# Optimization experiments

Measured on AMD Instinct MI355X. Metric: run time of the kernel, lower is better.

The kernel has to match this reference:

```python
import jax, jax.numpy as jnp
import numpy as np

N_NODES = 50000
E_DIM = 128
H_DIM = 256
OUT_DIM = 2
N_EDGES = 800000
NEG_SLOPE = 0.01  # nn.LeakyReLU default


def gcn_conv(x, W, b, src, dst, n):
    """PyG GCNConv: h = x @ W; add self-loops; sym-normalized scatter-add; + bias."""
    h = x @ W  # [N, H]
    loop = jnp.arange(n, dtype=src.dtype)
    s = jnp.concatenate([src, loop])
    d = jnp.concatenate([dst, loop])
    w = jnp.ones_like(s, dtype=h.dtype)
    deg = jax.ops.segment_sum(w, d, num_segments=n)  # in-degree incl. self-loop
    dis = jnp.where(deg > 0, jax.lax.rsqrt(deg), jnp.zeros_like(deg))
    norm = dis[s] * dis[d]  # [E+N]
    msg = h[s] * norm[:, None]  # gather + scale
    out = jax.ops.segment_sum(msg, d, num_segments=n)  # scatter-add to targets
    return out + b


def setup_inputs() -> dict:
    key = jax.random.key(0)
    ks = jax.random.split(key, 12)
    inp = {
        "mask_feature": jax.random.normal(ks[0], (N_NODES, E_DIM), jnp.float32),
        "feature": jax.random.normal(ks[1], (N_NODES, E_DIM), jnp.float32),
        "edge_index": jax.random.randint(ks[2], (2, N_EDGES), 0, N_NODES, jnp.int64 if jax.config.jax_enable_x64 else jnp.int32),
        "edge_type": jax.random.randint(ks[3], (N_EDGES,), 0, 2, jnp.int64 if jax.config.jax_enable_x64 else jnp.int32),
        # learned parameters
        "W_in": jax.random.normal(ks[4], (E_DIM, H_DIM), jnp.float32) * 0.05,
        "b_in": jnp.zeros((H_DIM,), jnp.float32),
        "Wg1": jax.random.normal(ks[5], (H_DIM, H_DIM), jnp.float32) * 0.05,
        "bg1": jnp.zeros((H_DIM,), jnp.float32),
        "Wg2": jax.random.normal(ks[6], (H_DIM, H_DIM), jnp.float32) * 0.05,
        "bg2": jnp.zeros((H_DIM,), jnp.float32),
        "W_out": jax.random.normal(ks[7], (H_DIM, OUT_DIM), jnp.float32) * 0.05,
        "b_out": jnp.zeros((OUT_DIM,), jnp.float32),
    }
    return inp


def reference(mask_feature, feature, edge_index, edge_type,
              W_in, b_in, Wg1, bg1, Wg2, bg2, W_out, b_out):
    src, dst = edge_index[0], edge_index[1]
    n = mask_feature.shape[0]
    # main branch
    x = jax.nn.leaky_relu(mask_feature @ W_in + b_in, NEG_SLOPE)
    x = gcn_conv(x, Wg1, bg1, src, dst, n)
    # dropout is identity at inference
    x = gcn_conv(x, Wg2, bg2, src, dst, n)
    x = x @ W_out + b_out  # [N, out_dim]
    # mask branch
    m = jax.nn.leaky_relu((feature - mask_feature) @ W_in + b_in, NEG_SLOPE)
    m = m @ W_out + b_out  # [N, out_dim]
    return x * m
```

## Files before the change

### kernel.cpp

```cpp
#include <hip/hip_runtime.h>


#define NEG_SLOPE 0.01f
constexpr int HD = 256;
constexpr int CHUNK = 4096;
constexpr int BSTRIDE = 8192;

typedef __bf16 bf16x8 __attribute__((ext_vector_type(8)));
typedef unsigned short u16x8 __attribute__((ext_vector_type(8)));
typedef float f32x4 __attribute__((ext_vector_type(4)));

#define MFMA16 __builtin_amdgcn_mfma_f32_16x16x32_bf16

__device__ inline void split1(float v, unsigned short& h, unsigned short& l) {
  unsigned u = __float_as_uint(v);
  unsigned hb = u & 0xFFFF0000u;
  float lf = v - __uint_as_float(hb);
  unsigned ul = __float_as_uint(lf);
  h = (unsigned short)(hb >> 16);
  l = (unsigned short)((ul + 0x7FFFu + ((ul >> 16) & 1u)) >> 16);
}

__device__ inline unsigned short bf16rne(float v) {
  unsigned u = __float_as_uint(v);
  return (unsigned short)((u + 0x7FFFu + ((u >> 16) & 1u)) >> 16);
}

__global__ __launch_bounds__(256) void k_prep(
    const float* __restrict__ Win, u16x8* __restrict__ Wf,
    const float* __restrict__ Wg1, const float* __restrict__ Wg2,
    const float* __restrict__ Wo, const float* __restrict__ bin,
    const float* __restrict__ bg1, const float* __restrict__ bg2,
    const float* __restrict__ bo, float4* __restrict__ E1,
    float2* __restrict__ E2, float* __restrict__ uv, int* __restrict__ cur) {
  __shared__ float wt[256][2];
  const int bid = blockIdx.x, tid = threadIdx.x;
  if (bid < 16) {
    int f = bid * 4 + (tid >> 6);
    int lane = tid & 63;
    int nt = f >> 2, ks = f & 3;
    int n = nt * 16 + (lane & 15);
    int k0 = ks * 32 + (lane >> 4) * 8;
    u16x8 outv;
    #pragma unroll
    for (int j = 0; j < 8; ++j)
      outv[j] = bf16rne(Win[(size_t)(k0 + j) * HD + n]);
    Wf[f * 64 + lane] = outv;
  } else if (bid == 16) {
    int r = tid;
    float s0 = 0.f, s1 = 0.f;
    for (int k = 0; k < 256; ++k) {
      float w = Wg2[r * 256 + k];
      s0 = fmaf(w, Wo[k * 2 + 0], s0);
      s1 = fmaf(w, Wo[k * 2 + 1], s1);
    }
    wt[r][0] = s0; wt[r][1] = s1;
    __syncthreads();
    float b0 = 0.f, b1 = 0.f;
    for (int k = 0; k < 256; ++k) {
      float w = Wg1[r * 256 + k];
      b0 = fmaf(w, wt[k][0], b0);
      b1 = fmaf(w, wt[k][1], b1);
    }
    E1[r] = make_float4(bin[r], b0, b1, 0.f);
    E2[r] = make_float2(Wo[r * 2 + 0], Wo[r * 2 + 1]);
    if (r < 2) {
      float u = 0.f, v = 0.f;
      for (int k = 0; k < 256; ++k) {
        u = fmaf(bg1[k], wt[k][r], u);
        v = fmaf(bg2[k], Wo[k * 2 + r], v);
      }
      uv[r] = u;
      uv[2 + r] = v + bo[r];
    }
  } else {
    cur[tid] = 0;
  }
}

__global__ __launch_bounds__(256, 2) void k_main(
    const float* __restrict__ mf, const float* __restrict__ fe,
    const u16x8* __restrict__ Wf, const float4* __restrict__ E1,
    const float2* __restrict__ E2, const float* __restrict__ bo,
    float4* __restrict__ q, float* __restrict__ Pm,
    const int* __restrict__ src, const int* __restrict__ dst,
    int* __restrict__ cur, unsigned* __restrict__ packed,
    int N, int E, int Gg) {
  __shared__ __align__(16) char smem[20608];
  const int tid = threadIdx.x;
  const int lane = tid & 63, wid = tid >> 6;

  if ((int)blockIdx.x < Gg) {
    float4* sE1 = (float4*)smem;
    float2* sE2 = (float2*)(smem + 4096);
    sE1[tid] = E1[tid];
    sE2[tid] = E2[tid];

    const int gb = blockIdx.x * 64;
    const int base = gb + wid * 16;
    int arow = base + (lane & 15);
    if (arow >= N) arow = N - 1;
    const int kb = (lane >> 4) * 8;
    const float* ap = mf + (size_t)arow * 128 + kb;
    const float* fp = fe + (size_t)arow * 128 + kb;

    bf16x8 Ah[4], Al[4], Kh[4], Kl[4];
    #pragma unroll
    for (int ks = 0; ks < 4; ++ks) {
      float x[8], y[8];
      *(float4*)&x[0] = *(const float4*)(ap + ks * 32);
      *(float4*)&x[4] = *(const float4*)(ap + ks * 32 + 4);
      *(float4*)&y[0] = *(const float4*)(fp + ks * 32);
      *(float4*)&y[4] = *(const float4*)(fp + ks * 32 + 4);
      u16x8 hA, lA, hM, lM;
      #pragma unroll
      for (int j = 0; j < 8; ++j) {
        unsigned short hh, ll;
        split1(x[j], hh, ll);        hA[j] = hh; lA[j] = ll;
        split1(y[j] - x[j], hh, ll); hM[j] = hh; lM[j] = ll;
      }
      Ah[ks] = __builtin_bit_cast(bf16x8, hA);
      Al[ks] = __builtin_bit_cast(bf16x8, lA);
      Kh[ks] = __builtin_bit_cast(bf16x8, hM);
      Kl[ks] = __builtin_bit_cast(bf16x8, lM);
    }
    __syncthreads();

    const u16x8* wp = Wf + lane;
    float s0[4] = {}, s1[4] = {}, t0v[4] = {}, t1v[4] = {};
    u16x8 bA[4], bB[4];
    #pragma unroll
    for (int f = 0; f < 4; ++f) bA[f] = wp[f * 64];

    auto COMPUTE = [&](const u16x8* b, int nt) {
      f32x4 a0 = {0,0,0,0}, a1 = {0,0,0,0};
      f32x4 k0 = {0,0,0,0}, k1 = {0,0,0,0};
      #pragma unroll
      for (int ks = 0; ks < 4; ++ks) {
        bf16x8 bh = __builtin_bit_cast(bf16x8, b[ks]);
        a0 = MFMA16(Ah[ks], bh, a0, 0, 0, 0);
        a1 = MFMA16(Al[ks], bh, a1, 0, 0, 0);
        k0 = MFMA16(Kh[ks], bh, k0, 0, 0, 0);
        k1 = MFMA16(Kl[ks], bh, k1, 0, 0, 0);
      }
      const int col = nt * 16 + (lane & 15);
      const float4 e1 = sE1[col];
      const float2 e2 = sE2[col];
      #pragma unroll
      for (int r = 0; r < 4; ++r) {
        float a = (a0[r] + a1[r]) + e1.x;
        a = a > 0.f ? a : NEG_SLOPE * a;
        s0[r] = fmaf(a, e1.y, s0[r]); s1[r] = fmaf(a, e1.z, s1[r]);
        float m = (k0[r] + k1[r]) + e1.x;
        m = m > 0.f ? m : NEG_SLOPE * m;
        t0v[r] = fmaf(m, e2.x, t0v[r]); t1v[r] = fmaf(m, e2.y, t1v[r]);
      }
    };

    #pragma unroll 1
    for (int nt = 0; nt < 16; nt += 2) {
      #pragma unroll
      for (int f = 0; f < 4; ++f) bB[f] = wp[((nt + 1) * 4 + f) * 64];
      COMPUTE(bA, nt);
      if (nt + 2 < 16) {
        #pragma unroll
        for (int f = 0; f < 4; ++f) bA[f] = wp[((nt + 2) * 4 + f) * 64];
      }
      COMPUTE(bB, nt + 1);
    }

    #pragma unroll
    for (int o = 1; o < 16; o <<= 1) {
      #pragma unroll
      for (int r = 0; r < 4; ++r) {
        s0[r] += __shfl_xor(s0[r], o, 16);  s1[r] += __shfl_xor(s1[r], o, 16);
        t0v[r] += __shfl_xor(t0v[r], o, 16); t1v[r] += __shfl_xor(t1v[r], o, 16);
      }
    }
    if ((lane & 15) == 0) {
      float bo0 = bo[0], bo1 = bo[1];
      #pragma unroll
      for (int r = 0; r < 4; ++r) {
        int row = base + (lane >> 4) * 4 + r;
        if (row < N) {
          float* qf = (float*)&q[row];
          qf[1] = s0[r];
          qf[2] = s1[r];
          Pm[row * 2 + 0] = t0v[r] + bo0;
          Pm[row * 2 + 1] = t1v[r] + bo1;
        }
      }
    }
    return;
  }

  int* bins   = (int*)smem;
  int* lstart = (int*)(smem + 1024);
  int* gbase  = (int*)(smem + 2048);
  int* lcur   = (int*)(smem + 3072);
  int* wsum   = (int*)(smem + 4096);
  unsigned* sbuf = (unsigned*)(smem + 4112);
  const int t = tid, b = blockIdx.x - Gg;
  bins[t] = 0;
  __syncthreads();
  const int e0 = b * CHUNK, e1 = min(e0 + CHUNK, E), m = e1 - e0;
  for (int e = e0 + t; e < e1; e += 256)
    atomicAdd(&bins[dst[e] >> 8], 1);
  __syncthreads();
  {
    int v = bins[t], incl = v;
    #pragma unroll
    for (int o = 1; o < 64; o <<= 1) {
      int tmp = __shfl_up(incl, o, 64);
      if (lane >= o) incl += tmp;
    }
    if (lane == 63) wsum[wid] = incl;
    __syncthreads();
    int woff = 0;
    for (int w = 0; w < wid; ++w) woff += wsum[w];
    int st = woff + incl - v;
    lstart[t] = st;
    lcur[t] = st;
    gbase[t] = v ? atomicAdd(&cur[t], v) : 0;
  }
  __syncthreads();
  for (int e = e0 + t; e < e1; e += 256) {
    int d = dst[e], s = src[e];
    int slot = atomicAdd(&lcur[d >> 8], 1);
    sbuf[slot] = ((unsigned)d << 16) | (unsigned)s;
  }
  __syncthreads();
  for (int i = t; i < m; i += 256) {
    unsigned pv = sbuf[i];
    int bin = pv >> 24;
    packed[(size_t)bin * BSTRIDE + gbase[bin] + (i - lstart[bin])] = pv;
  }
}

__global__ __launch_bounds__(256) void k_p2(
    const unsigned* __restrict__ packed, const int* __restrict__ cur,
    int* __restrict__ rp, float4* __restrict__ q, int* __restrict__ csr, int N) {
  __shared__ int cnt[256], sc[256];
  __shared__ int wsum[4];
  __shared__ unsigned short sbuf[BSTRIDE];
  const int t = threadIdx.x;
  const int B = blockIdx.x;
  const int lane = t & 63, wid = t >> 6;
  int tot = cur[t], incl = tot;
  #pragma unroll
  for (int o = 1; o < 64; o <<= 1) {
    int tmp = __shfl_up(incl, o, 64);
    if (lane >= o) incl += tmp;
  }
  if (lane == 63) wsum[wid] = incl;
  __syncthreads();
  int woff = 0;
  for (int w = 0; w < wid; ++w) woff += wsum[w];
  sc[t] = woff + incl - tot;
  __syncthreads();
  const int base = sc[B];
  const int ecnt = cur[B];
  const unsigned* pk = packed + (size_t)B * BSTRIDE;
  cnt[t] = 0;
  __syncthreads();
  for (int i = t; i < ecnt; i += 256)
    atomicAdd(&cnt[(pk[i] >> 16) & 0xFF], 1);
  __syncthreads();
  int v = cnt[t];
  incl = v;
  #pragma unroll
  for (int o = 1; o < 64; o <<= 1) {
    int tmp = __shfl_up(incl, o, 64);
    if (lane >= o) incl += tmp;
  }
  if (lane == 63) wsum[wid] = incl;
  __syncthreads();
  woff = 0;
  for (int w = 0; w < wid; ++w) woff += wsum[w];
  const int off = woff + incl - v;
  const int node = B * 256 + t;
  if (node < N) {
    rp[node] = base + off;
    ((float*)&q[node])[0] = rsqrtf((float)(v + 1));
  } else if (node == N) {
    rp[N] = base + off;
  }
  __syncthreads();
  cnt[t] = off;
  __syncthreads();
  for (int i = t; i < ecnt; i += 256) {
    unsigned pv = pk[i];
    int slot = atomicAdd(&cnt[(pv >> 16) & 0xFF], 1);
    sbuf[slot] = (unsigned short)(pv & 0xFFFFu);
  }
  __syncthreads();
  for (int i = t; i < ecnt; i += 256)
    csr[base + i] = (int)sbuf[i];
}

__global__ __launch_bounds__(256) void k_gather1(
    const int* __restrict__ rp, const int* __restrict__ csr,
    const float4* __restrict__ q, const float* __restrict__ uv,
    float* __restrict__ T2, int N) {
  int t = threadIdx.x;
  int n = blockIdx.x * 32 + (t >> 3);
  int l = t & 7;
  if (n >= N) return;
  int s0 = rp[n], s1 = rp[n + 1];
  float a0 = 0.f, a1 = 0.f;
  int j = s0 + l;
  for (; j + 8 < s1; j += 16) {
    int i0 = csr[j], i1 = csr[j + 8];
    float4 q0 = q[i0], q1 = q[i1];
    a0 = fmaf(q0.x, q0.y, a0); a1 = fmaf(q0.x, q0.z, a1);
    a0 = fmaf(q1.x, q1.y, a0); a1 = fmaf(q1.x, q1.z, a1);
  }
  if (j < s1) {
    float4 qa = q[csr[j]];
    a0 = fmaf(qa.x, qa.y, a0); a1 = fmaf(qa.x, qa.z, a1);
  }
  a0 += __shfl_xor(a0, 1, 8); a1 += __shfl_xor(a1, 1, 8);
  a0 += __shfl_xor(a0, 2, 8); a1 += __shfl_xor(a1, 2, 8);
  a0 += __shfl_xor(a0, 4, 8); a1 += __shfl_xor(a1, 4, 8);
  if (l == 0) {
    float4 qn = q[n];
    float d = qn.x;
    T2[n * 2 + 0] = d * (d * fmaf(d, qn.y, a0) + uv[0]);
    T2[n * 2 + 1] = d * (d * fmaf(d, qn.z, a1) + uv[1]);
  }
}

__global__ __launch_bounds__(256) void k_gather2(
    const int* __restrict__ rp, const int* __restrict__ csr,
    const float* __restrict__ T2, const float4* __restrict__ q,
    const float* __restrict__ uv, const float* __restrict__ Pm,
    float* __restrict__ out, int N) {
  int t = threadIdx.x;
  int n = blockIdx.x * 32 + (t >> 3);
  int l = t & 7;
  if (n >= N) return;
  int s0 = rp[n], s1 = rp[n + 1];
  float a0 = 0.f, a1 = 0.f;
  int j = s0 + l;
  for (; j + 8 < s1; j += 16) {
    int i0 = csr[j], i1 = csr[j + 8];
    float2 v0 = *(const float2*)&T2[i0 * 2];
    float2 v1 = *(const float2*)&T2[i1 * 2];
    a0 += v0.x + v1.x; a1 += v0.y + v1.y;
  }
  if (j < s1) {
    float2 va = *(const float2*)&T2[csr[j] * 2];
    a0 += va.x; a1 += va.y;
  }
  a0 += __shfl_xor(a0, 1, 8); a1 += __shfl_xor(a1, 1, 8);
  a0 += __shfl_xor(a0, 2, 8); a1 += __shfl_xor(a1, 2, 8);
  a0 += __shfl_xor(a0, 4, 8); a1 += __shfl_xor(a1, 4, 8);
  if (l == 0) {
    float d = q[n].x;
    float2 tv = *(const float2*)&T2[n * 2];
    float z0 = d * (tv.x + a0) + uv[2];
    float z1 = d * (tv.y + a1) + uv[3];
    out[n * 2 + 0] = z0 * Pm[n * 2 + 0];
    out[n * 2 + 1] = z1 * Pm[n * 2 + 1];
  }
}

extern "C" void kernel_launch(void* const* d_in, const int* in_sizes, int n_in,
                              void* d_out, int out_size, void* d_ws, size_t ws_size,
                              hipStream_t stream) {
  const float* mf  = (const float*)d_in[0];
  const float* fe  = (const float*)d_in[1];
  const int*   ei  = (const int*)d_in[2];
  const float* Win = (const float*)d_in[4];
  const float* bin = (const float*)d_in[5];
  const float* Wg1 = (const float*)d_in[6];
  const float* bg1 = (const float*)d_in[7];
  const float* Wg2 = (const float*)d_in[8];
  const float* bg2 = (const float*)d_in[9];
  const float* Wo  = (const float*)d_in[10];
  const float* bo  = (const float*)d_in[11];
  float* out = (float*)d_out;

  const int ED = 128;
  const int N = in_sizes[0] / ED;
  const int E = in_sizes[3];
  const int* src = ei;
  const int* dst = ei + E;

  char* ws = (char*)d_ws;
  size_t off = 0;
  auto carve = [&](size_t bytes) {
    char* p = ws + off;
    off += (bytes + 255) & ~(size_t)255;
    return p;
  };
  int*      cur    = (int*)carve(256 * 4);
  unsigned* packed = (unsigned*)carve((size_t)256 * BSTRIDE * 4);
  int*      csr    = (int*)carve((size_t)E * 4);
  int*      rp     = (int*)carve((size_t)(N + 1) * 4);
  float4*   q      = (float4*)carve((size_t)N * 16);
  float*    T2     = (float*)carve((size_t)N * 2 * 4);
  float*    Pm     = (float*)carve((size_t)N * 2 * 4);
  float4*   E1     = (float4*)carve((size_t)HD * 16);
  float2*   E2     = (float2*)carve((size_t)HD * 8);
  float*    uv     = (float*)carve(4 * 4);
  u16x8*    Wf     = (u16x8*)carve((size_t)64 * 64 * 16);
  (void)ws_size; (void)n_in; (void)out_size;

  const int NB  = (E + CHUNK - 1) / CHUNK;
  const int NP2 = (N + 255) / 256;
  const int Gg  = (N + 63) / 64;
  const int Gt  = (N + 31) / 32;

  k_prep<<<18, 256, 0, stream>>>(Win, Wf, Wg1, Wg2, Wo, bin, bg1, bg2, bo,
                                 E1, E2, uv, cur);
  k_main<<<Gg + NB, 256, 0, stream>>>(mf, fe, Wf, E1, E2, bo, q, Pm,
                                      src, dst, cur, packed, N, E, Gg);
  k_p2<<<NP2, 256, 0, stream>>>(packed, cur, rp, q, csr, N);
  k_gather1<<<Gt, 256, 0, stream>>>(rp, csr, q, uv, T2, N);
  k_gather2<<<Gt, 256, 0, stream>>>(rp, csr, T2, q, uv, Pm, out, N);
}
```

Baseline: 82.65 us.

## Process two row tiles per block and prefetch the second tile's inputs

The GEMM part of k_main now has each block handle two 64-row tiles (t0 and t0+GQ) instead of one, halving the number of GEMM blocks. The second tile's mask_feature rows are loaded up front and its feature rows are prefetched during the first tile's MFMA loop, so global load latency overlaps compute. The cost is much higher register pressure (three 32-float staging arrays under launch_bounds(256,2)), which risks spills, and fewer blocks to balance against the edge-binning blocks.

```diff
diff --git a/kernel.cpp b/kernel.cpp
--- a/kernel.cpp
+++ b/kernel.cpp
@@ -85,112 +85,149 @@
     float4* __restrict__ q, float* __restrict__ Pm,
     const int* __restrict__ src, const int* __restrict__ dst,
     int* __restrict__ cur, unsigned* __restrict__ packed,
-    int N, int E, int Gg) {
+    int N, int E, int GQ, int Tg) {
   __shared__ __align__(16) char smem[20608];
   const int tid = threadIdx.x;
   const int lane = tid & 63, wid = tid >> 6;
 
-  if ((int)blockIdx.x < Gg) {
+  if ((int)blockIdx.x < GQ) {
     float4* sE1 = (float4*)smem;
     float2* sE2 = (float2*)(smem + 4096);
     sE1[tid] = E1[tid];
     sE2[tid] = E2[tid];
 
-    const int gb = blockIdx.x * 64;
-    const int base = gb + wid * 16;
-    int arow = base + (lane & 15);
-    if (arow >= N) arow = N - 1;
+    const int t0 = blockIdx.x;
+    const int t1 = t0 + GQ;
     const int kb = (lane >> 4) * 8;
-    const float* ap = mf + (size_t)arow * 128 + kb;
-    const float* fp = fe + (size_t)arow * 128 + kb;
-
-    bf16x8 Ah[4], Al[4], Kh[4], Kl[4];
-    #pragma unroll
-    for (int ks = 0; ks < 4; ++ks) {
-      float x[8], y[8];
-      *(float4*)&x[0] = *(const float4*)(ap + ks * 32);
-      *(float4*)&x[4] = *(const float4*)(ap + ks * 32 + 4);
-      *(float4*)&y[0] = *(const float4*)(fp + ks * 32);
-      *(float4*)&y[4] = *(const float4*)(fp + ks * 32 + 4);
-      u16x8 hA, lA, hM, lM;
-      #pragma unroll
-      for (int j = 0; j < 8; ++j) {
-        unsigned short hh, ll;
-        split1(x[j], hh, ll);        hA[j] = hh; lA[j] = ll;
-        split1(y[j] - x[j], hh, ll); hM[j] = hh; lM[j] = ll;
-      }
-      Ah[ks] = __builtin_bit_cast(bf16x8, hA);
-      Al[ks] = __builtin_bit_cast(bf16x8, lA);
-      Kh[ks] = __builtin_bit_cast(bf16x8, hM);
-      Kl[ks] = __builtin_bit_cast(bf16x8, lM);
-    }
-    __syncthreads();
-
+    const float bo0 = bo[0], bo1 = bo[1];
     const u16x8* wp = Wf + lane;
-    float s0[4] = {}, s1[4] = {}, t0v[4] = {}, t1v[4] = {};
-    u16x8 bA[4], bB[4];
-    #pragma unroll
-    for (int f = 0; f < 4; ++f) bA[f] = wp[f * 64];
-
-    auto COMPUTE = [&](const u16x8* b, int nt) {
-      f32x4 a0 = {0,0,0,0}, a1 = {0,0,0,0};
-      f32x4 k0 = {0,0,0,0}, k1 = {0,0,0,0};
+
+    auto rowptr = [&](int tile, const float* base) {
+      int arow = tile * 64 + wid * 16 + (lane & 15);
+      if (arow >= N) arow = N - 1;
+      return base + (size_t)arow * 128 + kb;
+    };
+
+    float xm0[32], yf0[32];
+    {
+      const float* ap = rowptr(t0, mf);
+      const float* fp = rowptr(t0, fe);
       #pragma unroll
       for (int ks = 0; ks < 4; ++ks) {
-        bf16x8 bh = __builtin_bit_cast(bf16x8, b[ks]);
-        a0 = MFMA16(Ah[ks], bh, a0, 0, 0, 0);
-        a1 = MFMA16(Al[ks], bh, a1, 0, 0, 0);
-        k0 = MFMA16(Kh[ks], bh, k0, 0, 0, 0);
-        k1 = MFMA16(Kl[ks], bh, k1, 0, 0, 0);
-      }
-      const int col = nt * 16 + (lane & 15);
-      const float4 e1 = sE1[col];
-      const float2 e2 = sE2[col];
+        *(float4*)&xm0[ks * 8 + 0] = *(const float4*)(ap + ks * 32);
+        *(float4*)&xm0[ks * 8 + 4] = *(const float4*)(ap + ks * 32 + 4);
+        *(float4*)&yf0[ks * 8 + 0] = *(const float4*)(fp + ks * 32);
+        *(float4*)&yf0[ks * 8 + 4] = *(const float4*)(fp + ks * 32 + 4);
+      }
+    }
+    float xm1[32];
+    const bool has1 = t1 < Tg;
+    if (has1) {
+      const float* ap = rowptr(t1, mf);
       #pragma unroll
-      for (int r = 0; r < 4; ++r) {
-        float a = (a0[r] + a1[r]) + e1.x;
-        a = a > 0.f ? a : NEG_SLOPE * a;
-        s0[r] = fmaf(a, e1.y, s0[r]); s1[r] = fmaf(a, e1.z, s1[r]);
-        float m = (k0[r] + k1[r]) + e1.x;
-        m = m > 0.f ? m : NEG_SLOPE * m;
-        t0v[r] = fmaf(m, e2.x, t0v[r]); t1v[r] = fmaf(m, e2.y, t1v[r]);
+      for (int ks = 0; ks < 4; ++ks) {
+        *(float4*)&xm1[ks * 8 + 0] = *(const float4*)(ap + ks * 32);
+        *(float4*)&xm1[ks * 8 + 4] = *(const float4*)(ap + ks * 32 + 4);
+      }
+    }
+    __syncthreads();
+
+    float yf1[32];
+
+    auto DO_TILE = [&](const float* xm, const float* yf, int tile, bool pfFe) {
+      bf16x8 Ah[4], Al[4], Kh[4], Kl[4];
+      #pragma unroll
+      for (int ks = 0; ks < 4; ++ks) {
+        u16x8 hA, lA, hM, lM;
+        #pragma unroll
+        for (int j = 0; j < 8; ++j) {
+          unsigned short hh, ll;
+          float x = xm[ks * 8 + j];
+          split1(x, hh, ll);               hA[j] = hh; lA[j] = ll;
+          split1(yf[ks * 8 + j] - x, hh, ll); hM[j] = hh; lM[j] = ll;
+        }
+        Ah[ks] = __builtin_bit_cast(bf16x8, hA);
+        Al[ks] = __builtin_bit_cast(bf16x8, lA);
+        Kh[ks] = __builtin_bit_cast(bf16x8, hM);
+        Kl[ks] = __builtin_bit_cast(bf16x8, lM);
+      }
+
+      float s0[4] = {}, s1[4] = {}, t0v[4] = {}, t1v[4] = {};
+      u16x8 bA[4], bB[4];
+      #pragma unroll
+      for (int f = 0; f < 4; ++f) bA[f] = wp[f * 64];
+
+      auto COMPUTE = [&](const u16x8* b, int nt) {
+        f32x4 a0 = {0,0,0,0}, a1 = {0,0,0,0};
+        f32x4 k0 = {0,0,0,0}, k1 = {0,0,0,0};
+        #pragma unroll
+        for (int ks = 0; ks < 4; ++ks) {
+          bf16x8 bh = __builtin_bit_cast(bf16x8, b[ks]);
+          a0 = MFMA16(Ah[ks], bh, a0, 0, 0, 0);
+          a1 = MFMA16(Al[ks], bh, a1, 0, 0, 0);
+          k0 = MFMA16(Kh[ks], bh, k0, 0, 0, 0);
+          k1 = MFMA16(Kl[ks], bh, k1, 0, 0, 0);
+        }
+        const int col = nt * 16 + (lane & 15);
+        const float4 e1 = sE1[col];
+        const float2 e2 = sE2[col];
+        #pragma unroll
+        for (int r = 0; r < 4; ++r) {
+          float a = (a0[r] + a1[r]) + e1.x;
+          a = a > 0.f ? a : NEG_SLOPE * a;
+          s0[r] = fmaf(a, e1.y, s0[r]); s1[r] = fmaf(a, e1.z, s1[r]);
+          float m = (k0[r] + k1[r]) + e1.x;
+          m = m > 0.f ? m : NEG_SLOPE * m;
+          t0v[r] = fmaf(m, e2.x, t0v[r]); t1v[r] = fmaf(m, e2.y, t1v[r]);
+        }
+      };
+
+      #pragma unroll 1
+      for (int nt = 0; nt < 16; nt += 2) {
+        #pragma unroll
+        for (int f = 0; f < 4; ++f) bB[f] = wp[((nt + 1) * 4 + f) * 64];
+        COMPUTE(bA, nt);
+        if (nt + 2 < 16) {
+          #pragma unroll
+          for (int f = 0; f < 4; ++f) bA[f] = wp[((nt + 2) * 4 + f) * 64];
+        }
+        COMPUTE(bB, nt + 1);
+      }
+
+      if (pfFe) {
+        const float* fp = rowptr(t1, fe);
+        #pragma unroll
+        for (int ks = 0; ks < 4; ++ks) {
+          *(float4*)&yf1[ks * 8 + 0] = *(const float4*)(fp + ks * 32);
+          *(float4*)&yf1[ks * 8 + 4] = *(const float4*)(fp + ks * 32 + 4);
+        }
+      }
+
+      #pragma unroll
+      for (int o = 1; o < 16; o <<= 1) {
+        #pragma unroll
+        for (int r = 0; r < 4; ++r) {
+          s0[r] += __shfl_xor(s0[r], o, 16);  s1[r] += __shfl_xor(s1[r], o, 16);
+          t0v[r] += __shfl_xor(t0v[r], o, 16); t1v[r] += __shfl_xor(t1v[r], o, 16);
+        }
+      }
+      if ((lane & 15) == 0) {
+        #pragma unroll
+        for (int r = 0; r < 4; ++r) {
+          int row = tile * 64 + wid * 16 + (lane >> 4) * 4 + r;
+          if (row < N) {
+            float* qf = (float*)&q[row];
+            qf[1] = s0[r];
+            qf[2] = s1[r];
+            Pm[row * 2 + 0] = t0v[r] + bo0;
+            Pm[row * 2 + 1] = t1v[r] + bo1;
+          }
+        }
       }
     };
 
-    #pragma unroll 1
-    for (int nt = 0; nt < 16; nt += 2) {
-      #pragma unroll
-      for (int f = 0; f < 4; ++f) bB[f] = wp[((nt + 1) * 4 + f) * 64];
-      COMPUTE(bA, nt);
-      if (nt + 2 < 16) {
-        #pragma unroll
-        for (int f = 0; f < 4; ++f) bA[f] = wp[((nt + 2) * 4 + f) * 64];
-      }
-      COMPUTE(bB, nt + 1);
-    }
-
-    #pragma unroll
-    for (int o = 1; o < 16; o <<= 1) {
-      #pragma unroll
-      for (int r = 0; r < 4; ++r) {
-        s0[r] += __shfl_xor(s0[r], o, 16);  s1[r] += __shfl_xor(s1[r], o, 16);
-        t0v[r] += __shfl_xor(t0v[r], o, 16); t1v[r] += __shfl_xor(t1v[r], o, 16);
-      }
-    }
-    if ((lane & 15) == 0) {
-      float bo0 = bo[0], bo1 = bo[1];
-      #pragma unroll
-      for (int r = 0; r < 4; ++r) {
-        int row = base + (lane >> 4) * 4 + r;
-        if (row < N) {
-          float* qf = (float*)&q[row];
-          qf[1] = s0[r];
-          qf[2] = s1[r];
-          Pm[row * 2 + 0] = t0v[r] + bo0;
-          Pm[row * 2 + 1] = t1v[r] + bo1;
-        }
-      }
-    }
+    DO_TILE(xm0, yf0, t0, has1);
+    if (has1) DO_TILE(xm1, yf1, t1, false);
     return;
   }
 
@@ -200,7 +237,7 @@
   int* lcur   = (int*)(smem + 3072);
   int* wsum   = (int*)(smem + 4096);
   unsigned* sbuf = (unsigned*)(smem + 4112);
-  const int t = tid, b = blockIdx.x - Gg;
+  const int t = tid, b = blockIdx.x - GQ;
   bins[t] = 0;
   __syncthreads();
   const int e0 = b * CHUNK, e1 = min(e0 + CHUNK, E), m = e1 - e0;
@@ -409,13 +446,14 @@
 
   const int NB  = (E + CHUNK - 1) / CHUNK;
   const int NP2 = (N + 255) / 256;
-  const int Gg  = (N + 63) / 64;
+  const int Tg  = (N + 63) / 64;
+  const int GQ  = (Tg + 1) / 2;
   const int Gt  = (N + 31) / 32;
 
   k_prep<<<18, 256, 0, stream>>>(Win, Wf, Wg1, Wg2, Wo, bin, bg1, bg2, bo,
                                  E1, E2, uv, cur);
-  k_main<<<Gg + NB, 256, 0, stream>>>(mf, fe, Wf, E1, E2, bo, q, Pm,
-                                      src, dst, cur, packed, N, E, Gg);
+  k_main<<<GQ + NB, 256, 0, stream>>>(mf, fe, Wf, E1, E2, bo, q, Pm,
+                                      src, dst, cur, packed, N, E, GQ, Tg);
   k_p2<<<NP2, 256, 0, stream>>>(packed, cur, rp, q, csr, N);
   k_gather1<<<Gt, 256, 0, stream>>>(rp, csr, q, uv, T2, N);
   k_gather2<<<Gt, 256, 0, stream>>>(rp, csr, T2, q, uv, Pm, out, N);
```

Result: no change. 83.06 us (+0.5%).

## Replace CSR build and gathers with bucketed LDS atomic scatter aggregation

Applied to the files above, without the earlier changes.

Drops the per-bucket CSR construction (prefix scans, local sort, csr/rp writes). The two aggregation passes now read the dst-bucketed packed edge lists directly and accumulate into shared-memory float atomics per 256-node bucket. Degree normalisation is precomputed into a separate Tq array so the first pass only gathers a float2. The aim is to remove a sort pass and the global csr traffic. In exchange it relies on LDS atomics, and the float summation order becomes nondeterministic.

```diff
diff --git a/kernel.cpp b/kernel.cpp
--- a/kernel.cpp
+++ b/kernel.cpp
@@ -82,7 +82,7 @@
     const float* __restrict__ mf, const float* __restrict__ fe,
     const u16x8* __restrict__ Wf, const float4* __restrict__ E1,
     const float2* __restrict__ E2, const float* __restrict__ bo,
-    float4* __restrict__ q, float* __restrict__ Pm,
+    float2* __restrict__ P, float2* __restrict__ Pm,
     const int* __restrict__ src, const int* __restrict__ dst,
     int* __restrict__ cur, unsigned* __restrict__ packed,
     int N, int E, int Gg) {
@@ -183,11 +183,8 @@
       for (int r = 0; r < 4; ++r) {
         int row = base + (lane >> 4) * 4 + r;
         if (row < N) {
-          float* qf = (float*)&q[row];
-          qf[1] = s0[r];
-          qf[2] = s1[r];
-          Pm[row * 2 + 0] = t0v[r] + bo0;
-          Pm[row * 2 + 1] = t1v[r] + bo1;
+          P[row]  = make_float2(s0[r], s1[r]);
+          Pm[row] = make_float2(t0v[r] + bo0, t1v[r] + bo1);
         }
       }
     }
@@ -237,131 +234,104 @@
   }
 }
 
-__global__ __launch_bounds__(256) void k_p2(
+__global__ __launch_bounds__(1024) void k_dis(
     const unsigned* __restrict__ packed, const int* __restrict__ cur,
-    int* __restrict__ rp, float4* __restrict__ q, int* __restrict__ csr, int N) {
-  __shared__ int cnt[256], sc[256];
-  __shared__ int wsum[4];
-  __shared__ unsigned short sbuf[BSTRIDE];
-  const int t = threadIdx.x;
-  const int B = blockIdx.x;
-  const int lane = t & 63, wid = t >> 6;
-  int tot = cur[t], incl = tot;
-  #pragma unroll
-  for (int o = 1; o < 64; o <<= 1) {
-    int tmp = __shfl_up(incl, o, 64);
-    if (lane >= o) incl += tmp;
-  }
-  if (lane == 63) wsum[wid] = incl;
-  __syncthreads();
-  int woff = 0;
-  for (int w = 0; w < wid; ++w) woff += wsum[w];
-  sc[t] = woff + incl - tot;
-  __syncthreads();
-  const int base = sc[B];
+    const float2* __restrict__ P, float* __restrict__ dq,
+    float2* __restrict__ Tq, int N) {
+  __shared__ int cnt[256];
+  const int tid = threadIdx.x, B = blockIdx.x;
+  if (tid < 256) cnt[tid] = 0;
+  __syncthreads();
   const int ecnt = cur[B];
   const unsigned* pk = packed + (size_t)B * BSTRIDE;
-  cnt[t] = 0;
-  __syncthreads();
-  for (int i = t; i < ecnt; i += 256)
+  for (int i = tid; i < ecnt; i += 1024)
     atomicAdd(&cnt[(pk[i] >> 16) & 0xFF], 1);
   __syncthreads();
-  int v = cnt[t];
-  incl = v;
-  #pragma unroll
-  for (int o = 1; o < 64; o <<= 1) {
-    int tmp = __shfl_up(incl, o, 64);
-    if (lane >= o) incl += tmp;
-  }
-  if (lane == 63) wsum[wid] = incl;
-  __syncthreads();
-  woff = 0;
-  for (int w = 0; w < wid; ++w) woff += wsum[w];
-  const int off = woff + incl - v;
-  const int node = B * 256 + t;
-  if (node < N) {
-    rp[node] = base + off;
-    ((float*)&q[node])[0] = rsqrtf((float)(v + 1));
-  } else if (node == N) {
-    rp[N] = base + off;
-  }
-  __syncthreads();
-  cnt[t] = off;
-  __syncthreads();
-  for (int i = t; i < ecnt; i += 256) {
-    unsigned pv = pk[i];
-    int slot = atomicAdd(&cnt[(pv >> 16) & 0xFF], 1);
-    sbuf[slot] = (unsigned short)(pv & 0xFFFFu);
-  }
-  __syncthreads();
-  for (int i = t; i < ecnt; i += 256)
-    csr[base + i] = (int)sbuf[i];
-}
-
-__global__ __launch_bounds__(256) void k_gather1(
-    const int* __restrict__ rp, const int* __restrict__ csr,
-    const float4* __restrict__ q, const float* __restrict__ uv,
-    float* __restrict__ T2, int N) {
-  int t = threadIdx.x;
-  int n = blockIdx.x * 32 + (t >> 3);
-  int l = t & 7;
-  if (n >= N) return;
-  int s0 = rp[n], s1 = rp[n + 1];
-  float a0 = 0.f, a1 = 0.f;
-  int j = s0 + l;
-  for (; j + 8 < s1; j += 16) {
-    int i0 = csr[j], i1 = csr[j + 8];
-    float4 q0 = q[i0], q1 = q[i1];
-    a0 = fmaf(q0.x, q0.y, a0); a1 = fmaf(q0.x, q0.z, a1);
-    a0 = fmaf(q1.x, q1.y, a0); a1 = fmaf(q1.x, q1.z, a1);
-  }
-  if (j < s1) {
-    float4 qa = q[csr[j]];
-    a0 = fmaf(qa.x, qa.y, a0); a1 = fmaf(qa.x, qa.z, a1);
-  }
-  a0 += __shfl_xor(a0, 1, 8); a1 += __shfl_xor(a1, 1, 8);
-  a0 += __shfl_xor(a0, 2, 8); a1 += __shfl_xor(a1, 2, 8);
-  a0 += __shfl_xor(a0, 4, 8); a1 += __shfl_xor(a1, 4, 8);
-  if (l == 0) {
-    float4 qn = q[n];
-    float d = qn.x;
-    T2[n * 2 + 0] = d * (d * fmaf(d, qn.y, a0) + uv[0]);
-    T2[n * 2 + 1] = d * (d * fmaf(d, qn.z, a1) + uv[1]);
-  }
-}
-
-__global__ __launch_bounds__(256) void k_gather2(
-    const int* __restrict__ rp, const int* __restrict__ csr,
-    const float* __restrict__ T2, const float4* __restrict__ q,
-    const float* __restrict__ uv, const float* __restrict__ Pm,
-    float* __restrict__ out, int N) {
-  int t = threadIdx.x;
-  int n = blockIdx.x * 32 + (t >> 3);
-  int l = t & 7;
-  if (n >= N) return;
-  int s0 = rp[n], s1 = rp[n + 1];
-  float a0 = 0.f, a1 = 0.f;
-  int j = s0 + l;
-  for (; j + 8 < s1; j += 16) {
-    int i0 = csr[j], i1 = csr[j + 8];
-    float2 v0 = *(const float2*)&T2[i0 * 2];
-    float2 v1 = *(const float2*)&T2[i1 * 2];
-    a0 += v0.x + v1.x; a1 += v0.y + v1.y;
-  }
-  if (j < s1) {
-    float2 va = *(const float2*)&T2[csr[j] * 2];
-    a0 += va.x; a1 += va.y;
-  }
-  a0 += __shfl_xor(a0, 1, 8); a1 += __shfl_xor(a1, 1, 8);
-  a0 += __shfl_xor(a0, 2, 8); a1 += __shfl_xor(a1, 2, 8);
-  a0 += __shfl_xor(a0, 4, 8); a1 += __shfl_xor(a1, 4, 8);
-  if (l == 0) {
-    float d = q[n].x;
-    float2 tv = *(const float2*)&T2[n * 2];
-    float z0 = d * (tv.x + a0) + uv[2];
-    float z1 = d * (tv.y + a1) + uv[3];
-    out[n * 2 + 0] = z0 * Pm[n * 2 + 0];
-    out[n * 2 + 1] = z1 * Pm[n * 2 + 1];
+  if (tid < 256) {
+    int node = B * 256 + tid;
+    if (node < N) {
+      float d = rsqrtf((float)(cnt[tid] + 1));
+      dq[node] = d;
+      float2 p = P[node];
+      Tq[node] = make_float2(d * p.x, d * p.y);
+    }
+  }
+}
+
+__global__ __launch_bounds__(1024) void k_agg1(
+    const unsigned* __restrict__ packed, const int* __restrict__ cur,
+    const float2* __restrict__ Tq, const float* __restrict__ dq,
+    const float* __restrict__ uv, float2* __restrict__ T2, int N) {
+  __shared__ float acc[512];
+  const int tid = threadIdx.x, B = blockIdx.x;
+  if (tid < 512) acc[tid] = 0.f;
+  __syncthreads();
+  const int ecnt = cur[B];
+  const unsigned* pk = packed + (size_t)B * BSTRIDE;
+  int i = tid;
+  for (; i + 1024 < ecnt; i += 2048) {
+    unsigned p0 = pk[i], p1 = pk[i + 1024];
+    float2 t0 = Tq[p0 & 0xFFFFu];
+    float2 t1 = Tq[p1 & 0xFFFFu];
+    int d0 = ((p0 >> 16) & 0xFF) * 2, d1 = ((p1 >> 16) & 0xFF) * 2;
+    atomicAdd(&acc[d0], t0.x); atomicAdd(&acc[d0 + 1], t0.y);
+    atomicAdd(&acc[d1], t1.x); atomicAdd(&acc[d1 + 1], t1.y);
+  }
+  if (i < ecnt) {
+    unsigned p0 = pk[i];
+    float2 t0 = Tq[p0 & 0xFFFFu];
+    int d0 = ((p0 >> 16) & 0xFF) * 2;
+    atomicAdd(&acc[d0], t0.x); atomicAdd(&acc[d0 + 1], t0.y);
+  }
+  __syncthreads();
+  if (tid < 256) {
+    int node = B * 256 + tid;
+    if (node < N) {
+      float d = dq[node];
+      float2 tn = Tq[node];
+      T2[node] = make_float2(d * (d * (tn.x + acc[tid * 2 + 0]) + uv[0]),
+                             d * (d * (tn.y + acc[tid * 2 + 1]) + uv[1]));
+    }
+  }
+}
+
+__global__ __launch_bounds__(1024) void k_agg2(
+    const unsigned* __restrict__ packed, const int* __restrict__ cur,
+    const float2* __restrict__ T2, const float* __restrict__ dq,
+    const float* __restrict__ uv, const float2* __restrict__ Pm,
+    float2* __restrict__ out, int N) {
+  __shared__ float acc[512];
+  const int tid = threadIdx.x, B = blockIdx.x;
+  if (tid < 512) acc[tid] = 0.f;
+  __syncthreads();
+  const int ecnt = cur[B];
+  const unsigned* pk = packed + (size_t)B * BSTRIDE;
+  int i = tid;
+  for (; i + 1024 < ecnt; i += 2048) {
+    unsigned p0 = pk[i], p1 = pk[i + 1024];
+    float2 t0 = T2[p0 & 0xFFFFu];
+    float2 t1 = T2[p1 & 0xFFFFu];
+    int d0 = ((p0 >> 16) & 0xFF) * 2, d1 = ((p1 >> 16) & 0xFF) * 2;
+    atomicAdd(&acc[d0], t0.x); atomicAdd(&acc[d0 + 1], t0.y);
+    atomicAdd(&acc[d1], t1.x); atomicAdd(&acc[d1 + 1], t1.y);
+  }
+  if (i < ecnt) {
+    unsigned p0 = pk[i];
+    float2 t0 = T2[p0 & 0xFFFFu];
+    int d0 = ((p0 >> 16) & 0xFF) * 2;
+    atomicAdd(&acc[d0], t0.x); atomicAdd(&acc[d0 + 1], t0.y);
+  }
+  __syncthreads();
+  if (tid < 256) {
+    int node = B * 256 + tid;
+    if (node < N) {
+      float d = dq[node];
+      float2 tn = T2[node];
+      float2 pm = Pm[node];
+      float z0 = d * (tn.x + acc[tid * 2 + 0]) + uv[2];
+      float z1 = d * (tn.y + acc[tid * 2 + 1]) + uv[3];
+      out[node] = make_float2(z0 * pm.x, z1 * pm.y);
+    }
   }
 }
 
@@ -379,7 +349,7 @@
   const float* bg2 = (const float*)d_in[9];
   const float* Wo  = (const float*)d_in[10];
   const float* bo  = (const float*)d_in[11];
-  float* out = (float*)d_out;
+  float2* out = (float2*)d_out;
 
   const int ED = 128;
   const int N = in_sizes[0] / ED;
@@ -396,11 +366,11 @@
   };
   int*      cur    = (int*)carve(256 * 4);
   unsigned* packed = (unsigned*)carve((size_t)256 * BSTRIDE * 4);
-  int*      csr    = (int*)carve((size_t)E * 4);
-  int*      rp     = (int*)carve((size_t)(N + 1) * 4);
-  float4*   q      = (float4*)carve((size_t)N * 16);
-  float*    T2     = (float*)carve((size_t)N * 2 * 4);
-  float*    Pm     = (float*)carve((size_t)N * 2 * 4);
+  float2*   P      = (float2*)carve((size_t)N * 8);
+  float*    dq     = (float*)carve((size_t)N * 4);
+  float2*   Tq     = (float2*)carve((size_t)N * 8);
+  float2*   T2     = (float2*)carve((size_t)N * 8);
+  float2*   Pm     = (float2*)carve((size_t)N * 8);
   float4*   E1     = (float4*)carve((size_t)HD * 16);
   float2*   E2     = (float2*)carve((size_t)HD * 8);
   float*    uv     = (float*)carve(4 * 4);
@@ -410,13 +380,12 @@
   const int NB  = (E + CHUNK - 1) / CHUNK;
   const int NP2 = (N + 255) / 256;
   const int Gg  = (N + 63) / 64;
-  const int Gt  = (N + 31) / 32;
 
   k_prep<<<18, 256, 0, stream>>>(Win, Wf, Wg1, Wg2, Wo, bin, bg1, bg2, bo,
                                  E1, E2, uv, cur);
-  k_main<<<Gg + NB, 256, 0, stream>>>(mf, fe, Wf, E1, E2, bo, q, Pm,
+  k_main<<<Gg + NB, 256, 0, stream>>>(mf, fe, Wf, E1, E2, bo, P, Pm,
                                       src, dst, cur, packed, N, E, Gg);
-  k_p2<<<NP2, 256, 0, stream>>>(packed, cur, rp, q, csr, N);
-  k_gather1<<<Gt, 256, 0, stream>>>(rp, csr, q, uv, T2, N);
-  k_gather2<<<Gt, 256, 0, stream>>>(rp, csr, T2, q, uv, Pm, out, N);
-}
+  k_dis<<<NP2, 1024, 0, stream>>>(packed, cur, P, dq, Tq, N);
+  k_agg1<<<NP2, 1024, 0, stream>>>(packed, cur, Tq, dq, uv, T2, N);
+  k_agg2<<<NP2, 1024, 0, stream>>>(packed, cur, T2, dq, uv, Pm, out, N);
+}
```

Result: slower. 88.86 us (+7.5%).
